# Kernel optimization log

Measured on AMD Instinct MI355X. Metric: run time of the kernel, lower is better.

Reference implementation:

```python
import jax, jax.numpy as jnp
import numpy as np

N = 100000   # nodes
E = 1600000  # edges (avg degree 16)
H = 128      # hidden_dim
G = 256      # graphs in batch
IN = 2       # input feature dim (GCNConv(2, hidden_dim))


def setup_inputs() -> dict:
    key = jax.random.key(0)
    ks = jax.random.split(key, 12)
    def lin(k, fan_in, shape):
        # kaiming-uniform-ish init, scale irrelevant for correctness testing
        return jax.random.uniform(k, shape, jnp.float32, -1.0, 1.0) / np.sqrt(fan_in).astype(np.float32)
    return {
        "x": jax.random.normal(ks[0], (N, IN), jnp.float32),
        "edge_src": jax.random.randint(ks[1], (E,), 0, N, jnp.int32),
        "edge_dst": jax.random.randint(ks[2], (E,), 0, N, jnp.int32),
        "batch_ids": jnp.sort(jax.random.randint(ks[3], (N,), 0, G, jnp.int32)),
        "num_graphs": G,
        "W1": lin(ks[4], IN, (IN, H)), "b1": jnp.zeros((H,), jnp.float32),
        "W2": lin(ks[5], H, (H, H)),  "b2": jnp.zeros((H,), jnp.float32),
        "fc1_W": lin(ks[6], H, (H, H)), "fc1_b": lin(ks[7], H, (H,)),
        "fc2_W": lin(ks[8], H, (H, 1)), "fc2_b": lin(ks[9], H, (1,)),
    }


def gcn_layer(x, W, b, src, dst, n):
    # PyG GCNConv: add self-loops, symmetric deg^{-1/2} normalization,
    # linear transform, scatter-add aggregation, bias.
    h = x @ W                                                     # [N, H]
    deg = jax.ops.segment_sum(jnp.ones_like(src, jnp.float32), dst, num_segments=n) + 1.0  # +1 self-loop
    dinv = jax.lax.rsqrt(deg)                                     # [N]
    norm = dinv[src] * dinv[dst]                                  # [E]
    agg = jax.ops.segment_sum(h[src] * norm[:, None], dst, num_segments=n)  # [N, H]
    # self-loop contribution: deg_i^{-1/2} * deg_i^{-1/2} = 1/deg_i
    return agg + h * (1.0 / deg)[:, None] + b


def reference(x, edge_src, edge_dst, batch_ids, num_graphs,
              W1, b1, W2, b2, fc1_W, fc1_b, fc2_W, fc2_b):
    n = x.shape[0]
    h = jax.nn.relu(gcn_layer(x, W1, b1, edge_src, edge_dst, n))
    h = jax.nn.relu(gcn_layer(h, W2, b2, edge_src, edge_dst, n))
    # global_mean_pool
    sums = jax.ops.segment_sum(h, batch_ids, num_segments=num_graphs)            # [G, H]
    cnt = jax.ops.segment_sum(jnp.ones((n,), jnp.float32), batch_ids, num_segments=num_graphs)
    pooled = sums / jnp.maximum(cnt, 1.0)[:, None]
    h = jax.nn.relu(pooled @ fc1_W + fc1_b)
    return h @ fc2_W + fc2_b                                                     # [G, 1]
```

## Files before the change

### kernel.cpp

```cpp
#include <hip/hip_runtime.h>
#include <stdint.h>

#define HD 128
#define BSH 9
#define BNODES 512
#define PER 8
#define SCAP 256
#define BINBLK 512

typedef float f32x4 __attribute__((ext_vector_type(4)));
typedef float f32x2 __attribute__((ext_vector_type(2)));
typedef short s16x8 __attribute__((ext_vector_type(8)));

static inline int idiv(int a, int b) { return (a + b - 1) / b; }

__device__ __forceinline__ unsigned short f2b(float f) {
  unsigned u = __float_as_uint(f);
  return (unsigned short)((u + 0x7fffu + ((u >> 16) & 1u)) >> 16);
}

__global__ void __launch_bounds__(256) k_cnt(const int* __restrict__ edst,
                                             int* __restrict__ btot,
                                             int E, int NB, int chunk) {
  __shared__ int hist[512];
  int blk = blockIdx.x;
  for (int b = threadIdx.x; b < NB; b += 256) hist[b] = 0;
  __syncthreads();
  int s0 = blk * chunk, s1 = min(E, s0 + chunk);
  for (int k = s0 + threadIdx.x; k < s1; k += 256)
    atomicAdd(&hist[edst[k] >> BSH], 1);
  __syncthreads();
  for (int b = threadIdx.x; b < NB; b += 256) {
    int h = hist[b];
    if (h) atomicAdd(&btot[b], h);
  }
}

__global__ void __launch_bounds__(1024) k_bscan(const int* __restrict__ btot,
                                                int* __restrict__ bstart,
                                                int* __restrict__ gcur,
                                                float4* __restrict__ td,
                                                int NB, int E, int N) {
  __shared__ int sh[1024];
  int t = threadIdx.x;
  int a0 = (2 * t < NB) ? btot[2 * t] : 0;
  int a1 = (2 * t + 1 < NB) ? btot[2 * t + 1] : 0;
  int s = a0 + a1;
  sh[t] = s;
  __syncthreads();
  for (int off = 1; off < 1024; off <<= 1) {
    int add = (t >= off) ? sh[t - off] : 0;
    __syncthreads();
    sh[t] += add;
    __syncthreads();
  }
  int excl = sh[t] - s;
  if (2 * t < NB) { bstart[2 * t] = excl; gcur[2 * t] = excl; }
  if (2 * t + 1 < NB) { bstart[2 * t + 1] = excl + a0; gcur[2 * t + 1] = excl + a0; }
  if (t == 0) {
    bstart[NB] = E;
    td[N] = make_float4(0.f, 0.f, 0.f, 0.f);
  }
}

__global__ void __launch_bounds__(256) k_binscatter2(const int* __restrict__ esrc,
                                                     const int* __restrict__ edst,
                                                     int* __restrict__ gcur,
                                                     unsigned* __restrict__ recs,
                                                     int E, int NB, int chunk) {
  __shared__ int hist[512];
  int blk = blockIdx.x;
  for (int b = threadIdx.x; b < NB; b += 256) hist[b] = 0;
  __syncthreads();
  int s0 = blk * chunk, s1 = min(E, s0 + chunk);
  for (int k = s0 + threadIdx.x; k < s1; k += 256)
    atomicAdd(&hist[edst[k] >> BSH], 1);
  __syncthreads();
  for (int b = threadIdx.x; b < NB; b += 256) {
    int h = hist[b];
    hist[b] = h ? atomicAdd(&gcur[b], h) : 0;
  }
  __syncthreads();
  for (int k = s0 + threadIdx.x; k < s1; k += 256) {
    int d = edst[k], s = esrc[k];
    int b = d >> BSH;
    int pos = atomicAdd(&hist[b], 1);
    recs[pos] = ((unsigned)(d & (BNODES - 1)) << 23) | (unsigned)s;
  }
}

__global__ void __launch_bounds__(256) k_bucketsort(const unsigned* __restrict__ recs,
                                                    const int* __restrict__ bstart,
                                                    const float* __restrict__ x,
                                                    const int* __restrict__ bids,
                                                    unsigned* __restrict__ ssrc16,
                                                    int* __restrict__ row_start,
                                                    int* __restrict__ cnt,
                                                    float* __restrict__ dinv,
                                                    float2* __restrict__ xs,
                                                    int* __restrict__ gstart,
                                                    int NB, int N, int G) {
  __shared__ int count[BNODES], excl[BNODES], cur[BNODES], psum[64];
  int b = blockIdx.x;
  int t = threadIdx.x;
  for (int d = t; d < BNODES; d += 256) count[d] = 0;
  __syncthreads();
  int rs = bstart[b];
  int re = bstart[b + 1];
  int base_p = rs + b * BNODES;
  for (int k = rs + t; k < re; k += 256) atomicAdd(&count[recs[k] >> 23], 1);
  __syncthreads();
  if (t < 64) {
    int s = 0;
#pragma unroll
    for (int u = 0; u < 8; ++u) s += (count[t * 8 + u] + 1) & ~1;
    psum[t] = s;
  }
  __syncthreads();
  if (t == 0) {
    int run = 0;
    for (int d = 0; d < 64; ++d) { int v = psum[d]; psum[d] = run; run += v; }
  }
  __syncthreads();
  if (t < 64) {
    int run = psum[t];
#pragma unroll
    for (int u = 0; u < 8; ++u) {
      excl[t * 8 + u] = run;
      run += (count[t * 8 + u] + 1) & ~1;
    }
  }
  __syncthreads();
  for (int d = t; d < BNODES; d += 256) {
    int i = b * BNODES + d;
    if (i < N) {
      cnt[i] = count[d];
      row_start[i] = base_p + excl[d];
      if (count[d] & 1)
        ssrc16[base_p + excl[d] + count[d]] = (unsigned)N << 4;
      float di = rsqrtf((float)(count[d] + 1));
      dinv[i] = di;
      float2 xv = *(const float2*)&x[2 * i];
      xs[i] = make_float2(di * xv.x, di * xv.y);
      int g = bids[i];
      if (i == 0)
        for (int gg = 0; gg <= g; ++gg) gstart[gg] = 0;
      int gn = (i == N - 1) ? G : bids[i + 1];
      for (int gg = g + 1; gg <= gn; ++gg) gstart[gg] = i + 1;
    }
    cur[d] = excl[d];
  }
  __syncthreads();
  for (int k = rs + t; k < re; k += 256) {
    unsigned r = recs[k];
    int dl = r >> 23;
    int pos = base_p + atomicAdd(&cur[dl], 1);
    ssrc16[pos] = (r & 0x007fffffu) << 4;
  }
}

__global__ void k_aggx2(const int* __restrict__ row_start, const int* __restrict__ cnt,
                        const unsigned* __restrict__ ssrc16, const float2* __restrict__ xs,
                        const float* __restrict__ dinv, float4* __restrict__ td, int N) {
  int i = blockIdx.x * 256 + threadIdx.x;
  if (i >= N) return;
  int rs = row_start[i], re = rs + cnt[i];
  float a0 = 0.f, a1 = 0.f, b0 = 0.f, b1 = 0.f;
  int k = rs;
  for (; k + 3 < re; k += 4) {
    unsigned v0 = ssrc16[k] >> 4, v1 = ssrc16[k + 1] >> 4;
    unsigned v2 = ssrc16[k + 2] >> 4, v3 = ssrc16[k + 3] >> 4;
    float2 p0 = xs[v0], p1 = xs[v1], p2 = xs[v2], p3 = xs[v3];
    a0 += p0.x + p1.x; a1 += p0.y + p1.y;
    b0 += p2.x + p3.x; b1 += p2.y + p3.y;
  }
  for (; k < re; ++k) {
    float2 p = xs[ssrc16[k] >> 4];
    a0 += p.x; a1 += p.y;
  }
  a0 += b0; a1 += b1;
  float2 self = xs[i];
  float di = dinv[i];
  td[i] = make_float4(di * (a0 + self.x), di * (a1 + self.y), di, 0.f);
}

__global__ void __launch_bounds__(256) k_aggh(
    const int* __restrict__ row_start, const int* __restrict__ cnt,
    const unsigned* __restrict__ ssrc16, const float4* __restrict__ td,
    const float* __restrict__ W1, const float* __restrict__ b1,
    unsigned* __restrict__ m_b, int N) {
  __shared__ float4 sbuf[4][SCAP];
  int wave = threadIdx.x >> 6;
  int lane = threadIdx.x & 63;
  int wid = blockIdx.x * 4 + wave;
  int i0 = wid * PER;
  if (i0 >= N) return;
  int nn = min(N - i0, PER);
  int hl = lane >> 5;
  int fq = (lane & 31) * 4;
  f32x4 w0 = *(const f32x4*)&W1[fq];
  f32x4 w1 = *(const f32x4*)&W1[HD + fq];
  f32x4 bb = *(const f32x4*)&b1[fq];
  int mydeg = (lane < nn) ? cnt[i0 + lane] : 0;
  float4 mytd = (lane < nn) ? td[i0 + lane] : make_float4(0.f, 0.f, 0.f, 0.f);
  int mx = __float_as_int(mytd.x), my = __float_as_int(mytd.y), mz = __float_as_int(mytd.z);
  int mypad = (mydeg + 1) & ~1;
  int total = 0;
#pragma unroll
  for (int u = 0; u < PER; ++u) total += __builtin_amdgcn_readlane(mypad, u);
  int rs0 = __builtin_amdgcn_readfirstlane(row_start[i0]);
  const char* tdc = (const char*)td;
  bool staged = (total <= SCAP);
  if (staged) {
#pragma unroll
    for (int w = 0; w < SCAP / 64; ++w) {
      int sl = w * 64 + lane;
      if (sl < total) {
        unsigned off = ssrc16[rs0 + sl];
        sbuf[wave][sl] = *(const float4*)(tdc + off);
      }
    }
  }
  int k = 0;
  const f32x4 zero4 = {0.f, 0.f, 0.f, 0.f};
  for (int node = 0; node < nn; ++node) {
    int deg = __builtin_amdgcn_readlane(mydeg, node);
    int np = (deg + 1) >> 1;
    f32x4 acc = zero4;
    if (staged) {
#pragma unroll 2
      for (int p = 0; p < np; ++p) {
        float4 t = sbuf[wave][k + 2 * p + hl];
        f32x4 h = f32x4{t.y, t.y, t.y, t.y} * w1 + bb;
        h = f32x4{t.x, t.x, t.x, t.x} * w0 + h;
        h = __builtin_elementwise_max(h, zero4);
        acc = f32x4{t.z, t.z, t.z, t.z} * h + acc;
      }
    } else {
      for (int p = 0; p < np; ++p) {
        unsigned off = ssrc16[rs0 + k + 2 * p + hl];
        float4 t = *(const float4*)(tdc + off);
        f32x4 h = f32x4{t.y, t.y, t.y, t.y} * w1 + bb;
        h = f32x4{t.x, t.x, t.x, t.x} * w0 + h;
        h = __builtin_elementwise_max(h, zero4);
        acc = f32x4{t.z, t.z, t.z, t.z} * h + acc;
      }
    }
    k += np * 2;
    f32x4 tot;
#pragma unroll
    for (int c = 0; c < 4; ++c) tot[c] = acc[c] + __shfl_xor(acc[c], 32);
    float tx = __int_as_float(__builtin_amdgcn_readlane(mx, node));
    float ty = __int_as_float(__builtin_amdgcn_readlane(my, node));
    float tz = __int_as_float(__builtin_amdgcn_readlane(mz, node));
    f32x4 h = f32x4{ty, ty, ty, ty} * w1 + bb;
    h = f32x4{tx, tx, tx, tx} * w0 + h;
    h = __builtin_elementwise_max(h, zero4);
    f32x4 r = f32x4{tz, tz, tz, tz} * h + tot;
    float v0 = (hl ? r[2] : r[0]) * tz;
    float v1 = (hl ? r[3] : r[1]) * tz;
    int j = hl ? (2 * (lane - 32) + 1) : (2 * lane);
    m_b[(unsigned)(i0 + node) * 64 + j] = ((unsigned)f2b(v1) << 16) | f2b(v0);
  }
}

__global__ void k_w2t(const float* __restrict__ W2, unsigned* __restrict__ w2f,
                      int* __restrict__ btot, int NB) {
  int f = blockIdx.x * 256 + threadIdx.x;
  if (f < NB) btot[f] = 0;
  if (f >= 2048) return;
  int c = f >> 8, s = (f >> 6) & 3, lane = f & 63;
  int col = c * 16 + (lane & 15);
  int kb = s * 32 + (lane >> 4) * 8;
  unsigned hi4[4], lo4[4];
#pragma unroll
  for (int j = 0; j < 4; ++j) {
    float w0 = W2[(kb + 2 * j) * HD + col];
    float w1 = W2[(kb + 2 * j + 1) * HD + col];
    unsigned short h0 = f2b(w0), h1 = f2b(w1);
    float r0 = w0 - __uint_as_float((unsigned)h0 << 16);
    float r1 = w1 - __uint_as_float((unsigned)h1 << 16);
    unsigned short l0 = f2b(r0), l1 = f2b(r1);
    hi4[j] = ((unsigned)h1 << 16) | h0;
    lo4[j] = ((unsigned)l1 << 16) | l0;
  }
  *(uint4*)&w2f[f * 4] = make_uint4(hi4[0], hi4[1], hi4[2], hi4[3]);
  *(uint4*)&w2f[8192 + f * 4] = make_uint4(lo4[0], lo4[1], lo4[2], lo4[3]);
}

__global__ void __launch_bounds__(256) k_t2pool(
    const unsigned* __restrict__ m_b, const unsigned* __restrict__ w2f,
    const float* __restrict__ b2, const int* __restrict__ gstart,
    const float* __restrict__ fc1W, const float* __restrict__ fc1b,
    const float* __restrict__ fc2W, const float* __restrict__ fc2b,
    float* __restrict__ out, int N, int G) {
  __shared__ unsigned W[16384];
  __shared__ float pool[16][HD];
  __shared__ float ps[HD];
  __shared__ float rsh[HD];
  int g = blockIdx.x;
  for (int u = threadIdx.x; u < 4096; u += 256)
    *(uint4*)&W[u * 4] = *(const uint4*)&w2f[u * 4];
  for (int u = threadIdx.x; u < 16 * HD; u += 256) ((float*)pool)[u] = 0.f;
  const int lane = threadIdx.x & 63;
  const int wave = threadIdx.x >> 6;
  const int col = lane & 15;
  const int kg = lane >> 4;
  float bb[8];
#pragma unroll
  for (int c = 0; c < 8; ++c) bb[c] = b2[c * 16 + col];
  int s0 = gstart[g], e0 = gstart[g + 1];
  int ntiles = (e0 - s0 + 15) >> 4;
  float pacc[8];
#pragma unroll
  for (int c = 0; c < 8; ++c) pacc[c] = 0.f;
  __syncthreads();
  for (int tile = wave; tile < ntiles; tile += 4) {
    int rbase = s0 + tile * 16;
    int arow = rbase + col;
    if (arow >= N) arow = N - 1;
    f32x4 acc[8];
#pragma unroll
    for (int c = 0; c < 8; ++c) acc[c] = f32x4{0.f, 0.f, 0.f, 0.f};
#pragma unroll
    for (int s = 0; s < 4; ++s) {
      uint4 av = *(const uint4*)&m_b[((size_t)arow << 6) + s * 16 + kg * 4];
      s16x8 A = *(s16x8*)&av;
#pragma unroll
      for (int c = 0; c < 8; ++c) {
        int f = (c * 4 + s) * 64 + lane;
        s16x8 Bh = *(s16x8*)&W[f * 4];
        s16x8 Bl = *(s16x8*)&W[8192 + f * 4];
        acc[c] = __builtin_amdgcn_mfma_f32_16x16x32_bf16(A, Bh, acc[c], 0, 0, 0);
        acc[c] = __builtin_amdgcn_mfma_f32_16x16x32_bf16(A, Bl, acc[c], 0, 0, 0);
      }
    }
    int orow = rbase + kg * 4;
#pragma unroll
    for (int c = 0; c < 8; ++c) {
#pragma unroll
      for (int r = 0; r < 4; ++r) {
        if (orow + r < e0) pacc[c] += fmaxf(acc[c][r] + bb[c], 0.f);
      }
    }
  }
#pragma unroll
  for (int c = 0; c < 8; ++c) pool[wave * 4 + kg][c * 16 + col] = pacc[c];
  __syncthreads();
  int j = threadIdx.x;
  if (j < HD) {
    float a = 0.f;
#pragma unroll
    for (int r = 0; r < 16; ++r) a += pool[r][j];
    float cg = (float)(e0 - s0);
    cg = cg < 1.f ? 1.f : cg;
    ps[j] = a / cg;
  }
  __syncthreads();
  if (j < HD) {
    float a = fc1b[j];
#pragma unroll 4
    for (int k = 0; k < HD; ++k) a = fmaf(ps[k], fc1W[k * HD + j], a);
    rsh[j] = fmaxf(a, 0.f) * fc2W[j];
  }
  __syncthreads();
  for (int off = 64; off > 0; off >>= 1) {
    if (j < off) rsh[j] += rsh[j + off];
    __syncthreads();
  }
  if (j == 0) out[g] = rsh[0] + fc2b[0];
}

extern "C" void kernel_launch(void* const* d_in, const int* in_sizes, int n_in,
                              void* d_out, int out_size, void* d_ws, size_t ws_size,
                              hipStream_t stream) {
  const float* x    = (const float*)d_in[0];
  const int* esrc   = (const int*)d_in[1];
  const int* edst   = (const int*)d_in[2];
  const int* bids   = (const int*)d_in[3];
  const float* W1   = (const float*)d_in[5];
  const float* b1   = (const float*)d_in[6];
  const float* W2   = (const float*)d_in[7];
  const float* b2   = (const float*)d_in[8];
  const float* fc1W = (const float*)d_in[9];
  const float* fc1b = (const float*)d_in[10];
  const float* fc2W = (const float*)d_in[11];
  const float* fc2b = (const float*)d_in[12];
  float* out = (float*)d_out;

  const int N = in_sizes[0] / 2;
  const int E = in_sizes[1];
  const int G = out_size;

  const int NB = idiv(N, BNODES);
  const int chunk = idiv(E, BINBLK);

  char* w = (char*)d_ws;
  size_t o = 0;
  auto take = [&](size_t b) -> char* {
    char* p = w + o;
    o = (o + b + 255) & ~(size_t)255;
    return p;
  };
  int*      btot      = (int*)     take((size_t)NB * 4);
  int*      bstart    = (int*)     take((size_t)(NB + 1) * 4);
  int*      gcur      = (int*)     take((size_t)NB * 4);
  unsigned* recs      = (unsigned*)take((size_t)E * 4);
  unsigned* ssrc16    = (unsigned*)take((size_t)(E + (size_t)NB * BNODES + 128) * 4);
  int*      cnt       = (int*)     take((size_t)N * 4);
  int*      row_start = (int*)     take((size_t)N * 4);
  float*    dinv      = (float*)   take((size_t)N * 4);
  float*    xs        = (float*)   take((size_t)N * 8);
  float*    td        = (float*)   take((size_t)(N + 1) * 16);
  int*      gstart    = (int*)     take((size_t)(G + 1) * 4);
  unsigned* m_b       = (unsigned*)take((size_t)N * 64 * 4);
  unsigned* w2f       = (unsigned*)take(16384 * 4);

  k_w2t<<<8, 256, 0, stream>>>(W2, w2f, btot, NB);
  k_cnt<<<BINBLK, 256, 0, stream>>>(edst, btot, E, NB, chunk);
  k_bscan<<<1, 1024, 0, stream>>>(btot, bstart, gcur, (float4*)td, NB, E, N);
  k_binscatter2<<<BINBLK, 256, 0, stream>>>(esrc, edst, gcur, recs, E, NB, chunk);
  k_bucketsort<<<NB, 256, 0, stream>>>(recs, bstart, x, bids, ssrc16, row_start,
                                       cnt, dinv, (float2*)xs, gstart, NB, N, G);
  k_aggx2<<<idiv(N, 256), 256, 0, stream>>>(row_start, cnt, ssrc16, (const float2*)xs,
                                            dinv, (float4*)td, N);
  int waves = idiv(N, PER);
  k_aggh<<<idiv(waves, 4), 256, 0, stream>>>(row_start, cnt, ssrc16, (const float4*)td,
                                             W1, b1, m_b, N);
  k_t2pool<<<G, 256, 0, stream>>>(m_b, w2f, b2, gstart, fc1W, fc1b, fc2W, fc2b, out, N, G);
}
```

Before: 141.5 us.

## Replace atomic bin offsets with block-by-bin count matrix scan for edge binning

```diff
diff --git a/kernel.cpp b/kernel.cpp
--- a/kernel.cpp
+++ b/kernel.cpp
@@ -2,11 +2,11 @@
 #include <stdint.h>
 
 #define HD 128
-#define BSH 9
-#define BNODES 512
+#define BSH 8
+#define BNODES 256
 #define PER 8
 #define SCAP 256
-#define BINBLK 512
+#define BINBLK 256
 
 typedef float f32x4 __attribute__((ext_vector_type(4)));
 typedef float f32x2 __attribute__((ext_vector_type(2)));
@@ -19,34 +19,38 @@
   return (unsigned short)((u + 0x7fffu + ((u >> 16) & 1u)) >> 16);
 }
 
-__global__ void __launch_bounds__(256) k_cnt(const int* __restrict__ edst,
-                                             int* __restrict__ btot,
-                                             int E, int NB, int chunk) {
+__global__ void __launch_bounds__(256) k_bincount(const int* __restrict__ edst,
+                                                  int* __restrict__ cntm,
+                                                  int E, int NB, int chunk) {
   __shared__ int hist[512];
   int blk = blockIdx.x;
-  for (int b = threadIdx.x; b < NB; b += 256) hist[b] = 0;
+  for (int b = threadIdx.x; b < 512; b += 256) hist[b] = 0;
   __syncthreads();
   int s0 = blk * chunk, s1 = min(E, s0 + chunk);
   for (int k = s0 + threadIdx.x; k < s1; k += 256)
     atomicAdd(&hist[edst[k] >> BSH], 1);
   __syncthreads();
-  for (int b = threadIdx.x; b < NB; b += 256) {
-    int h = hist[b];
-    if (h) atomicAdd(&btot[b], h);
-  }
-}
-
-__global__ void __launch_bounds__(1024) k_bscan(const int* __restrict__ btot,
-                                                int* __restrict__ bstart,
-                                                int* __restrict__ gcur,
-                                                float4* __restrict__ td,
-                                                int NB, int E, int N) {
+  for (int b = threadIdx.x; b < NB; b += 256)
+    cntm[(size_t)b * BINBLK + blk] = hist[b];
+}
+
+__global__ void k_scan1(const int* __restrict__ cnt, int* __restrict__ part, int N) {
+  __shared__ int sh[256];
+  int t = threadIdx.x;
+  int base = blockIdx.x * 1024 + t * 4;
+  int s = 0;
+#pragma unroll
+  for (int u = 0; u < 4; ++u) { int idx = base + u; if (idx < N) s += cnt[idx]; }
+  sh[t] = s; __syncthreads();
+  for (int off = 128; off > 0; off >>= 1) { if (t < off) sh[t] += sh[t + off]; __syncthreads(); }
+  if (t == 0) part[blockIdx.x] = sh[0];
+}
+
+__global__ void k_scan2(int* part, int nb) {
   __shared__ int sh[1024];
   int t = threadIdx.x;
-  int a0 = (2 * t < NB) ? btot[2 * t] : 0;
-  int a1 = (2 * t + 1 < NB) ? btot[2 * t + 1] : 0;
-  int s = a0 + a1;
-  sh[t] = s;
+  int v = (t < nb) ? part[t] : 0;
+  sh[t] = v;
   __syncthreads();
   for (int off = 1; off < 1024; off <<= 1) {
     int add = (t >= off) ? sh[t - off] : 0;
@@ -54,43 +58,56 @@
     sh[t] += add;
     __syncthreads();
   }
-  int excl = sh[t] - s;
-  if (2 * t < NB) { bstart[2 * t] = excl; gcur[2 * t] = excl; }
-  if (2 * t + 1 < NB) { bstart[2 * t + 1] = excl + a0; gcur[2 * t + 1] = excl + a0; }
-  if (t == 0) {
-    bstart[NB] = E;
-    td[N] = make_float4(0.f, 0.f, 0.f, 0.f);
-  }
-}
-
-__global__ void __launch_bounds__(256) k_binscatter2(const int* __restrict__ esrc,
-                                                     const int* __restrict__ edst,
-                                                     int* __restrict__ gcur,
-                                                     unsigned* __restrict__ recs,
-                                                     int E, int NB, int chunk) {
-  __shared__ int hist[512];
+  if (t < nb) part[t] = sh[t] - v;
+}
+
+__global__ void k_scan3(const int* __restrict__ cnt, const int* __restrict__ part,
+                        int* __restrict__ out, int N) {
+  __shared__ int sa[256], sb[256];
+  int t = threadIdx.x;
+  int base = blockIdx.x * 1024 + t * 4;
+  int v[4]; int s = 0;
+#pragma unroll
+  for (int u = 0; u < 4; ++u) { int idx = base + u; v[u] = (idx < N) ? cnt[idx] : 0; s += v[u]; }
+  sa[t] = s; __syncthreads();
+  int* cur = sa; int* nxt = sb;
+  for (int off = 1; off < 256; off <<= 1) {
+    int val = cur[t] + ((t >= off) ? cur[t - off] : 0);
+    nxt[t] = val; __syncthreads();
+    int* tmp = cur; cur = nxt; nxt = tmp;
+  }
+  int excl = cur[t] - s + part[blockIdx.x];
+#pragma unroll
+  for (int u = 0; u < 4; ++u) {
+    int idx = base + u;
+    if (idx < N) { out[idx] = excl; excl += v[u]; }
+  }
+}
+
+__global__ void k_sent(float4* __restrict__ td, int N) {
+  if (threadIdx.x == 0) td[N] = make_float4(0.f, 0.f, 0.f, 0.f);
+}
+
+__global__ void __launch_bounds__(256) k_binscatter(const int* __restrict__ esrc,
+                                                    const int* __restrict__ edst,
+                                                    const int* __restrict__ scanM,
+                                                    unsigned* __restrict__ recs,
+                                                    int E, int NB, int chunk) {
+  __shared__ int cur[512];
   int blk = blockIdx.x;
-  for (int b = threadIdx.x; b < NB; b += 256) hist[b] = 0;
+  for (int b = threadIdx.x; b < NB; b += 256) cur[b] = scanM[(size_t)b * BINBLK + blk];
   __syncthreads();
   int s0 = blk * chunk, s1 = min(E, s0 + chunk);
-  for (int k = s0 + threadIdx.x; k < s1; k += 256)
-    atomicAdd(&hist[edst[k] >> BSH], 1);
-  __syncthreads();
-  for (int b = threadIdx.x; b < NB; b += 256) {
-    int h = hist[b];
-    hist[b] = h ? atomicAdd(&gcur[b], h) : 0;
-  }
-  __syncthreads();
   for (int k = s0 + threadIdx.x; k < s1; k += 256) {
     int d = edst[k], s = esrc[k];
     int b = d >> BSH;
-    int pos = atomicAdd(&hist[b], 1);
+    int pos = atomicAdd(&cur[b], 1);
     recs[pos] = ((unsigned)(d & (BNODES - 1)) << 23) | (unsigned)s;
   }
 }
 
 __global__ void __launch_bounds__(256) k_bucketsort(const unsigned* __restrict__ recs,
-                                                    const int* __restrict__ bstart,
+                                                    const int* __restrict__ scanM,
                                                     const float* __restrict__ x,
                                                     const int* __restrict__ bids,
                                                     unsigned* __restrict__ ssrc16,
@@ -99,18 +116,18 @@
                                                     float* __restrict__ dinv,
                                                     float2* __restrict__ xs,
                                                     int* __restrict__ gstart,
-                                                    int NB, int N, int G) {
-  __shared__ int count[BNODES], excl[BNODES], cur[BNODES], psum[64];
+                                                    int NB, int N, int G, int E) {
+  __shared__ int count[BNODES], excl[BNODES], cur[BNODES], psum[32];
   int b = blockIdx.x;
   int t = threadIdx.x;
-  for (int d = t; d < BNODES; d += 256) count[d] = 0;
-  __syncthreads();
-  int rs = bstart[b];
-  int re = bstart[b + 1];
+  count[t] = 0;
+  __syncthreads();
+  int rs = scanM[(size_t)b * BINBLK];
+  int re = (b == NB - 1) ? E : scanM[(size_t)(b + 1) * BINBLK];
   int base_p = rs + b * BNODES;
   for (int k = rs + t; k < re; k += 256) atomicAdd(&count[recs[k] >> 23], 1);
   __syncthreads();
-  if (t < 64) {
+  if (t < 32) {
     int s = 0;
 #pragma unroll
     for (int u = 0; u < 8; ++u) s += (count[t * 8 + u] + 1) & ~1;
@@ -119,10 +136,10 @@
   __syncthreads();
   if (t == 0) {
     int run = 0;
-    for (int d = 0; d < 64; ++d) { int v = psum[d]; psum[d] = run; run += v; }
-  }
-  __syncthreads();
-  if (t < 64) {
+    for (int d = 0; d < 32; ++d) { int v = psum[d]; psum[d] = run; run += v; }
+  }
+  __syncthreads();
+  if (t < 32) {
     int run = psum[t];
 #pragma unroll
     for (int u = 0; u < 8; ++u) {
@@ -131,7 +148,8 @@
     }
   }
   __syncthreads();
-  for (int d = t; d < BNODES; d += 256) {
+  {
+    int d = t;
     int i = b * BNODES + d;
     if (i < N) {
       cnt[i] = count[d];
@@ -202,13 +220,14 @@
   f32x4 w1 = *(const f32x4*)&W1[HD + fq];
   f32x4 bb = *(const f32x4*)&b1[fq];
   int mydeg = (lane < nn) ? cnt[i0 + lane] : 0;
+  int myrow = (lane < nn) ? row_start[i0 + lane] : 0;
   float4 mytd = (lane < nn) ? td[i0 + lane] : make_float4(0.f, 0.f, 0.f, 0.f);
   int mx = __float_as_int(mytd.x), my = __float_as_int(mytd.y), mz = __float_as_int(mytd.z);
-  int mypad = (mydeg + 1) & ~1;
-  int total = 0;
-#pragma unroll
-  for (int u = 0; u < PER; ++u) total += __builtin_amdgcn_readlane(mypad, u);
-  int rs0 = __builtin_amdgcn_readfirstlane(row_start[i0]);
+  int rs0 = __builtin_amdgcn_readfirstlane(myrow);
+  int last = nn - 1;
+  int rsEnd = __builtin_amdgcn_readlane(myrow, last) +
+              ((__builtin_amdgcn_readlane(mydeg, last) + 1) & ~1);
+  int total = rsEnd - rs0;
   const char* tdc = (const char*)td;
   bool staged = (total <= SCAP);
   if (staged) {
@@ -264,10 +283,8 @@
   }
 }
 
-__global__ void k_w2t(const float* __restrict__ W2, unsigned* __restrict__ w2f,
-                      int* __restrict__ btot, int NB) {
+__global__ void k_w2t(const float* __restrict__ W2, unsigned* __restrict__ w2f) {
   int f = blockIdx.x * 256 + threadIdx.x;
-  if (f < NB) btot[f] = 0;
   if (f >= 2048) return;
   int c = f >> 8, s = (f >> 6) & 3, lane = f & 63;
   int col = c * 16 + (lane & 15);
@@ -393,6 +410,7 @@
   const int G = out_size;
 
   const int NB = idiv(N, BNODES);
+  const int M = NB * BINBLK;
   const int chunk = idiv(E, BINBLK);
 
   char* w = (char*)d_ws;
@@ -402,11 +420,11 @@
     o = (o + b + 255) & ~(size_t)255;
     return p;
   };
-  int*      btot      = (int*)     take((size_t)NB * 4);
-  int*      bstart    = (int*)     take((size_t)(NB + 1) * 4);
-  int*      gcur      = (int*)     take((size_t)NB * 4);
+  int*      cntm      = (int*)     take((size_t)M * 4);
+  int*      scanM     = (int*)     take((size_t)M * 4);
+  int*      part      = (int*)     take(4096);
   unsigned* recs      = (unsigned*)take((size_t)E * 4);
-  unsigned* ssrc16    = (unsigned*)take((size_t)(E + (size_t)NB * BNODES + 128) * 4);
+  unsigned* ssrc16    = (unsigned*)take((size_t)(E + N + 256) * 4);
   int*      cnt       = (int*)     take((size_t)N * 4);
   int*      row_start = (int*)     take((size_t)N * 4);
   float*    dinv      = (float*)   take((size_t)N * 4);
@@ -416,12 +434,16 @@
   unsigned* m_b       = (unsigned*)take((size_t)N * 64 * 4);
   unsigned* w2f       = (unsigned*)take(16384 * 4);
 
-  k_w2t<<<8, 256, 0, stream>>>(W2, w2f, btot, NB);
-  k_cnt<<<BINBLK, 256, 0, stream>>>(edst, btot, E, NB, chunk);
-  k_bscan<<<1, 1024, 0, stream>>>(btot, bstart, gcur, (float4*)td, NB, E, N);
-  k_binscatter2<<<BINBLK, 256, 0, stream>>>(esrc, edst, gcur, recs, E, NB, chunk);
-  k_bucketsort<<<NB, 256, 0, stream>>>(recs, bstart, x, bids, ssrc16, row_start,
-                                       cnt, dinv, (float2*)xs, gstart, NB, N, G);
+  int nbM = idiv(M, 1024);
+  k_w2t<<<8, 256, 0, stream>>>(W2, w2f);
+  k_sent<<<1, 64, 0, stream>>>((float4*)td, N);
+  k_bincount<<<BINBLK, 256, 0, stream>>>(edst, cntm, E, NB, chunk);
+  k_scan1<<<nbM, 256, 0, stream>>>(cntm, part, M);
+  k_scan2<<<1, 1024, 0, stream>>>(part, nbM);
+  k_scan3<<<nbM, 256, 0, stream>>>(cntm, part, scanM, M);
+  k_binscatter<<<BINBLK, 256, 0, stream>>>(esrc, edst, scanM, recs, E, NB, chunk);
+  k_bucketsort<<<NB, 256, 0, stream>>>(recs, scanM, x, bids, ssrc16, row_start,
+                                       cnt, dinv, (float2*)xs, gstart, NB, N, G, E);
   k_aggx2<<<idiv(N, 256), 256, 0, stream>>>(row_start, cnt, ssrc16, (const float2*)xs,
                                             dinv, (float4*)td, N);
   int waves = idiv(N, PER);
```

After: 127.3 us. 10.1% less time.
